# Kernel tuning notes

Hardware: AMD Instinct MI355X
Metric: run time of the kernel (lower is better)

The kernel has to match this reference:

```python
import jax, jax.numpy as jnp
import numpy as np

H = 256  # hidden_size
B = 8192  # batch
S = 1024  # seq_length


def setup_inputs() -> dict:
    key = jax.random.key(0)
    ks = jax.random.split(key, 12)
    lim_g = 1.0 / np.sqrt(1 + H)  # torch Linear default init bound, fan_in = 1+H
    lim_o = 1.0 / np.sqrt(H)
    def lin(k, out_dim, in_dim, lim):
        kw, kb = jax.random.split(k)
        W = jax.random.uniform(kw, (out_dim, in_dim), jnp.float32, -lim, lim)
        b = jax.random.uniform(kb, (out_dim,), jnp.float32, -lim, lim)
        return W, b
    Wf, bf = lin(ks[0], H, 1 + H, lim_g)
    Wi, bi = lin(ks[1], H, 1 + H, lim_g)
    Wc, bc = lin(ks[2], H, 1 + H, lim_g)
    Wo, bo = lin(ks[3], H, 1 + H, lim_g)
    Wout, bout = lin(ks[4], 1, H, lim_o)
    x = jax.random.normal(ks[5], (B, S), jnp.float32)
    return {"x": x, "Wf": Wf, "bf": bf, "Wi": Wi, "bi": bi,
            "Wc": Wc, "bc": bc, "Wo": Wo, "bo": bo,
            "Wout": Wout, "bout": bout}


def reference(x, Wf, bf, Wi, bi, Wc, bc, Wo, bo, Wout, bout):
    B_, S_ = x.shape
    H_ = Wf.shape[0]
    # Fuse the four gate linears into one GEMM per step (same math):
    Wall = jnp.concatenate([Wf, Wi, Wc, Wo], axis=0)      # [4H, 1+H]
    ball = jnp.concatenate([bf, bi, bc, bo], axis=0)      # [4H]

    def step(carry, xt):
        h, c = carry                                       # [B,H], [B,H]
        conc = jnp.concatenate([xt[:, None], h], axis=1)   # [B, 1+H]
        g = conc @ Wall.T + ball                           # [B, 4H]
        f, i, cs, o = jnp.split(g, 4, axis=1)
        c = jax.nn.sigmoid(f) * c + jax.nn.sigmoid(i) * jnp.tanh(cs)
        h = jax.nn.sigmoid(o) * jnp.tanh(c)
        return (h, c), None

    h0 = jnp.zeros((B_, H_), x.dtype)
    c0 = jnp.zeros((B_, H_), x.dtype)
    (h, _), _ = jax.lax.scan(step, (h0, c0), x.T)          # scan over seq axis
    out = h @ Wout.T + bout                                # [B, 1]
    return out.squeeze(-1)                                 # [B]
```

## Files before the change

kernel.cpp:

```cpp
#include <hip/hip_runtime.h>
#include <hip/hip_fp16.h>


typedef _Float16 f16x8 __attribute__((ext_vector_type(8)));
typedef float f32x4 __attribute__((ext_vector_type(4)));
typedef unsigned int u32;
typedef unsigned short u16;

#define WINT_OFF 0u
#define W0B_OFF  524288u
#define FLAG_OFF 528384u
#define PUB_OFF  1048576u

static __device__ __forceinline__ float fast_exp2(float x) {
#if __has_builtin(__builtin_amdgcn_exp2f)
  return __builtin_amdgcn_exp2f(x);
#else
  return exp2f(x);
#endif
}
static __device__ __forceinline__ float fast_rcp(float x) {
#if __has_builtin(__builtin_amdgcn_rcpf)
  return __builtin_amdgcn_rcpf(x);
#else
  return 1.0f / x;
#endif
}
static __device__ __forceinline__ u16 f16b(float f) {
  union { _Float16 h; u16 u; } cv; cv.h = (_Float16)f; return cv.u;
}
static __device__ __forceinline__ float h2f(u16 u) {
  union { u16 u; _Float16 h; } cv; cv.u = u; return (float)cv.h;
}
static __device__ __forceinline__ u16* pub_base(u16* pub, int set, int par,
                                                int pid, int half) {
  return pub + ((size_t)(((set * 2 + par) * 128 + pid) * 2 + half) << 12);
}

__global__ void lstm_prep(const float* __restrict__ Wf, const float* __restrict__ Wi,
                          const float* __restrict__ Wc, const float* __restrict__ Wo,
                          const float* __restrict__ bf_, const float* __restrict__ bi_,
                          const float* __restrict__ bc_, const float* __restrict__ bo_,
                          u16* __restrict__ Wint, u32* __restrict__ w0b) {
  int n = blockIdx.x;
  int k = threadIdx.x;
  int g = n >> 8, j = n & 255;
  const float* Ws = (g == 0) ? Wf : (g == 1) ? Wi : (g == 2) ? Wc : Wo;
  const float scale = (g == 2) ? 2.88539008f : 1.44269504f;
  Wint[n * 256 + k] = f16b(Ws[j * 257 + 1 + k] * scale);
  if (k == 0) {
    const float* bs = (g == 0) ? bf_ : (g == 1) ? bi_ : (g == 2) ? bc_ : bo_;
    w0b[n] = (u32)f16b(Ws[j * 257] * scale) | ((u32)f16b(bs[j] * scale) << 16);
  }
}

__global__ void lstm_zero(uint4* __restrict__ pub4, uint4* __restrict__ flags4,
                          float* __restrict__ out, const float* __restrict__ bout) {
  int idx = blockIdx.x * 256 + threadIdx.x;
  uint4 z = uint4{0, 0, 0, 0};
  if (idx < 131072) pub4[idx] = z;
  else if (idx < 262144) pub4[idx + 131072] = z;
  else if (idx < 264192) flags4[idx - 262144] = z;
  else { int o = idx - 264192; if (o < 8192) out[o] = bout[0]; }
}

__global__ __launch_bounds__(512, 2) void lstm_main(
    const u16* __restrict__ Wint, const u32* __restrict__ w0b,
    const float* __restrict__ x, const float* __restrict__ Wout,
    float* __restrict__ out, u16* __restrict__ pub, int* __restrict__ flags) {

  __shared__ __align__(16) u16 stg[2][2][4096];

  const int tid  = threadIdx.x;
  const int wv   = tid >> 6;
  const int lane = tid & 63;
  const int l15  = lane & 15;
  const int quad = lane >> 4;
  const int B    = blockIdx.x;
  const int mi   = (B >> 3) & 1;
  const int peer = B ^ 8;
  const int pid  = (B & 7) | ((B >> 4) << 3);
  const int rows0 = pid * 64;

  f16x8 wfrag[4][8];
#pragma unroll
  for (int g = 0; g < 4; ++g)
#pragma unroll
    for (int hm = 0; hm < 2; ++hm)
#pragma unroll
      for (int ktl = 0; ktl < 4; ++ktl) {
        int kbase = (hm == 0 ? mi : 1 - mi) * 128 + ktl * 32;
        wfrag[g][hm * 4 + ktl] = *(const f16x8*)(Wint +
            (size_t)(g * 256 + mi * 128 + wv * 16 + l15) * 256 + kbase + quad * 8);
      }
  float w0f[4][4], bsf[4][4];
#pragma unroll
  for (int g = 0; g < 4; ++g) {
    uint4 wv4 = *(const uint4*)(w0b + g * 256 + mi * 128 + wv * 16 + quad * 4);
    u32 pka[4] = {wv4.x, wv4.y, wv4.z, wv4.w};
#pragma unroll
    for (int r = 0; r < 4; ++r) {
      w0f[g][r] = h2f((u16)pka[r]);
      bsf[g][r] = h2f((u16)(pka[r] >> 16));
    }
  }

#pragma unroll
  for (int i = 0; i < 4; ++i) ((uint4*)stg)[tid + i * 512] = uint4{0, 0, 0, 0};

  float cst[2][2][4];
#pragma unroll
  for (int s = 0; s < 2; ++s)
#pragma unroll
    for (int bt = 0; bt < 2; ++bt)
#pragma unroll
      for (int r = 0; r < 4; ++r) cst[s][bt][r] = 0.0f;

  const float* xq = x + (size_t)rows0 * 1024;
  float xcur[2][2];
#pragma unroll
  for (int s = 0; s < 2; ++s)
#pragma unroll
    for (int bt = 0; bt < 2; ++bt)
      xcur[s][bt] = xq[(size_t)(s * 32 + bt * 16 + l15) * 1024];

  int* const myflag = flags + B * 32;
  int* const pfl    = flags + peer * 32;

  __syncthreads();

#pragma unroll 1
  for (int t = 0; t < 1024; ++t) {
#pragma unroll
    for (int s = 0; s < 2; ++s) {
      f32x4 acc[4][2];
#pragma unroll
      for (int g = 0; g < 4; ++g)
#pragma unroll
        for (int r = 0; r < 4; ++r) {
          acc[g][0][r] = xcur[s][0] * w0f[g][r] + bsf[g][r];
          acc[g][1][r] = xcur[s][1] * w0f[g][r] + bsf[g][r];
        }
#pragma unroll
      for (int bt = 0; bt < 2; ++bt)
        xcur[s][bt] = xq[(size_t)(s * 32 + bt * 16 + l15) * 1024 + ((t + 1) & 1023)];

#pragma unroll
      for (int hm = 0; hm < 2; ++hm)
#pragma unroll
        for (int ktl = 0; ktl < 4; ++ktl) {
          f16x8 bb[2];
#pragma unroll
          for (int bt = 0; bt < 2; ++bt) {
            int b = bt * 16 + l15;
            int cp = (ktl * 4 + quad) ^ (b & 15);
            bb[bt] = *(const f16x8*)(&stg[s][hm][0] + b * 128 + cp * 8);
          }
#pragma unroll
          for (int g = 0; g < 4; ++g)
#pragma unroll
            for (int bt = 0; bt < 2; ++bt)
              acc[g][bt] = __builtin_amdgcn_mfma_f32_16x16x32_f16(
                  wfrag[g][hm * 4 + ktl], bb[bt], acc[g][bt], 0, 0, 0);
        }

      const int tn = (s == 0) ? t : t + 1;
      if (tn < 1024) {
        while (__hip_atomic_load(pfl + (s ^ 1) * 16, __ATOMIC_RELAXED,
                                 __HIP_MEMORY_SCOPE_AGENT) < tn)
          __builtin_amdgcn_s_sleep(1);
        const u16* srcO = pub_base(pub, s ^ 1, tn & 1, pid, mi);
        const u16* srcP = pub_base(pub, s ^ 1, tn & 1, pid, 1 - mi);
        __builtin_amdgcn_global_load_lds(
            (const __attribute__((address_space(1))) u32*)(srcO + wv * 512 + lane * 8),
            (__attribute__((address_space(3))) u32*)(&stg[s ^ 1][0][wv * 512]), 16, 0, 0);
        __builtin_amdgcn_global_load_lds(
            (const __attribute__((address_space(1))) u32*)(srcP + wv * 512 + lane * 8),
            (__attribute__((address_space(3))) u32*)(&stg[s ^ 1][1][wv * 512]), 16, 0, 0);
      }

      u16* pb = pub_base(pub, s, (t + 1) & 1, pid, mi);
#pragma unroll
      for (int bt = 0; bt < 2; ++bt) {
        int b = bt * 16 + l15;
        u32 lo, hi;
        {
          float h0, h1, h2, h3;
#pragma unroll
          for (int r = 0; r < 4; ++r) {
            float fg = acc[0][bt][r], ig = acc[1][bt][r];
            float cg = acc[2][bt][r], og = acc[3][bt][r];
            float sf  = fast_rcp(1.0f + fast_exp2(-fg));
            float C   = fast_exp2(cg);
            float Ei  = fast_exp2(-ig);
            float itv = (C - 1.0f) * fast_rcp((1.0f + Ei) * (C + 1.0f));
            float c_  = sf * cst[s][bt][r] + itv;
            cst[s][bt][r] = c_;
            float C2  = fast_exp2(2.88539008f * c_);
            float th  = 1.0f - 2.0f * fast_rcp(1.0f + C2);
            float so  = fast_rcp(1.0f + fast_exp2(-og));
            float hv  = so * th;
            if (r == 0) h0 = hv; else if (r == 1) h1 = hv;
            else if (r == 2) h2 = hv; else h3 = hv;
          }
          lo = (u32)f16b(h0) | ((u32)f16b(h1) << 16);
          hi = (u32)f16b(h2) | ((u32)f16b(h3) << 16);
        }
        int c16 = wv * 2 + (quad >> 1);
        int cp  = c16 ^ (b & 15);
        *(uint2*)(pb + b * 128 + cp * 8 + (quad & 1) * 4) = uint2{lo, hi};
      }

      __syncthreads();
      if (tid == 0)
        __hip_atomic_store(myflag + s * 16, t + 1, __ATOMIC_RELAXED,
                           __HIP_MEMORY_SCOPE_AGENT);
    }
  }

  if (tid < 64) {
    int s = tid >> 5, b = tid & 31;
    const u16* pbase = pub_base(pub, s, 0, pid, mi);
    float a = 0.0f;
#pragma unroll
    for (int c = 0; c < 16; ++c) {
      f16x8 hv = *(const f16x8*)(pbase + b * 128 + ((c ^ (b & 15)) * 8));
#pragma unroll
      for (int e = 0; e < 8; ++e) a += (float)hv[e] * Wout[mi * 128 + c * 8 + e];
    }
    atomicAdd(&out[rows0 + s * 32 + b], a);
  }
}

extern "C" void kernel_launch(void* const* d_in, const int* in_sizes, int n_in,
                              void* d_out, int out_size, void* d_ws, size_t ws_size,
                              hipStream_t stream) {
  const float* x    = (const float*)d_in[0];
  const float* Wf   = (const float*)d_in[1];
  const float* bf_  = (const float*)d_in[2];
  const float* Wi   = (const float*)d_in[3];
  const float* bi_  = (const float*)d_in[4];
  const float* Wc   = (const float*)d_in[5];
  const float* bc_  = (const float*)d_in[6];
  const float* Wo   = (const float*)d_in[7];
  const float* bo_  = (const float*)d_in[8];
  const float* Wout = (const float*)d_in[9];
  const float* bout = (const float*)d_in[10];

  u16* Wint  = (u16*)((char*)d_ws + WINT_OFF);
  u32* w0b   = (u32*)((char*)d_ws + W0B_OFF);
  int* flags = (int*)((char*)d_ws + FLAG_OFF);
  u16* pub   = (u16*)((char*)d_ws + PUB_OFF);

  lstm_prep<<<1024, 256, 0, stream>>>(Wf, Wi, Wc, Wo, bf_, bi_, bc_, bo_, Wint, w0b);
  lstm_zero<<<1064, 256, 0, stream>>>((uint4*)pub, (uint4*)flags, (float*)d_out, bout);
  lstm_main<<<256, 512, 0, stream>>>(Wint, w0b, x, Wout, (float*)d_out, pub, flags);
}
```

Baseline: 4.704 ms.

## Split waves into MFMA and elementwise groups to overlap recurrent step phases

Result: slower. 5.439 ms (+15.6%).

```diff
diff --git a/kernel.cpp b/kernel.cpp
--- a/kernel.cpp
+++ b/kernel.cpp
@@ -69,13 +69,14 @@
     const float* __restrict__ x, const float* __restrict__ Wout,
     float* __restrict__ out, u16* __restrict__ pub, int* __restrict__ flags) {
 
-  __shared__ __align__(16) u16 stg[2][2][4096];
+  __shared__ __align__(16) u16 stg[2][2][2][4096];
 
   const int tid  = threadIdx.x;
   const int wv   = tid >> 6;
   const int lane = tid & 63;
   const int l15  = lane & 15;
   const int quad = lane >> 4;
+  const int grp  = (wv & 1) ^ ((wv >> 2) & 1);
   const int B    = blockIdx.x;
   const int mi   = (B >> 3) & 1;
   const int peer = B ^ 8;
@@ -106,7 +107,7 @@
   }
 
 #pragma unroll
-  for (int i = 0; i < 4; ++i) ((uint4*)stg)[tid + i * 512] = uint4{0, 0, 0, 0};
+  for (int i = 0; i < 8; ++i) ((uint4*)stg)[tid + i * 512] = uint4{0, 0, 0, 0};
 
   float cst[2][2][4];
 #pragma unroll
@@ -115,6 +116,8 @@
     for (int bt = 0; bt < 2; ++bt)
 #pragma unroll
       for (int r = 0; r < 4; ++r) cst[s][bt][r] = 0.0f;
+
+  f32x4 acc[4][2];
 
   const float* xq = x + (size_t)rows0 * 1024;
   float xcur[2][2];
@@ -129,94 +132,149 @@
 
   __syncthreads();
 
+#define DO_K(S, T, LEAD) do {                                                  \
+    const int par_ = (T) & 1;                                                  \
+    if (LEAD) {                                                                \
+      while (__hip_atomic_load(pfl + (S) * 16, __ATOMIC_RELAXED,               \
+                               __HIP_MEMORY_SCOPE_AGENT) < (T))                \
+        __builtin_amdgcn_s_sleep(1);                                           \
+      const u16* srcP_ = pub_base(pub, (S), par_, pid, 1 - mi);                \
+      u16* dst_ = &stg[S][par_][1][0];                                         \
+      _Pragma("unroll")                                                        \
+      for (int i_ = 0; i_ < 8; ++i_)                                           \
+        __builtin_amdgcn_global_load_lds(                                      \
+            (const __attribute__((address_space(1))) u32*)(srcP_ + i_ * 512 + lane * 8), \
+            (__attribute__((address_space(3))) u32*)(dst_ + i_ * 512), 16, 0, 0); \
+      __builtin_amdgcn_sched_barrier(0);                                       \
+    }                                                                          \
+    _Pragma("unroll")                                                          \
+    for (int g_ = 0; g_ < 4; ++g_)                                             \
+      _Pragma("unroll")                                                        \
+      for (int r_ = 0; r_ < 4; ++r_) {                                         \
+        acc[g_][0][r_] = xcur[S][0] * w0f[g_][r_] + bsf[g_][r_];               \
+        acc[g_][1][r_] = xcur[S][1] * w0f[g_][r_] + bsf[g_][r_];               \
+      }                                                                        \
+    _Pragma("unroll")                                                          \
+    for (int ktl_ = 0; ktl_ < 4; ++ktl_) {                                     \
+      f16x8 bb_[2];                                                            \
+      _Pragma("unroll")                                                        \
+      for (int bt_ = 0; bt_ < 2; ++bt_) {                                      \
+        int b_ = bt_ * 16 + l15;                                               \
+        int cp_ = (ktl_ * 4 + quad) ^ (b_ & 15);                               \
+        bb_[bt_] = *(const f16x8*)(&stg[S][par_][0][0] + b_ * 128 + cp_ * 8);  \
+      }                                                                        \
+      _Pragma("unroll")                                                        \
+      for (int g_ = 0; g_ < 4; ++g_)                                           \
+        _Pragma("unroll")                                                      \
+        for (int bt_ = 0; bt_ < 2; ++bt_)                                      \
+          acc[g_][bt_] = __builtin_amdgcn_mfma_f32_16x16x32_f16(               \
+              wfrag[g_][ktl_], bb_[bt_], acc[g_][bt_], 0, 0, 0);               \
+    }                                                                          \
+    if (LEAD) {                                                                \
+      asm volatile("s_waitcnt vmcnt(0)" ::: "memory");                         \
+      __builtin_amdgcn_sched_barrier(0);                                       \
+    }                                                                          \
+    _Pragma("unroll")                                                          \
+    for (int ktl_ = 0; ktl_ < 4; ++ktl_) {                                     \
+      f16x8 bb_[2];                                                            \
+      _Pragma("unroll")                                                        \
+      for (int bt_ = 0; bt_ < 2; ++bt_) {                                      \
+        int b_ = bt_ * 16 + l15;                                               \
+        int cp_ = (ktl_ * 4 + quad) ^ (b_ & 15);                               \
+        bb_[bt_] = *(const f16x8*)(&stg[S][par_][1][0] + b_ * 128 + cp_ * 8);  \
+      }                                                                        \
+      _Pragma("unroll")                                                        \
+      for (int g_ = 0; g_ < 4; ++g_)                                           \
+        _Pragma("unroll")                                                      \
+        for (int bt_ = 0; bt_ < 2; ++bt_)                                      \
+          acc[g_][bt_] = __builtin_amdgcn_mfma_f32_16x16x32_f16(               \
+              wfrag[g_][4 + ktl_], bb_[bt_], acc[g_][bt_], 0, 0, 0);           \
+    }                                                                          \
+  } while (0)
+
+#define DO_EW(S, TEW) do {                                                     \
+    const int parn_ = ((TEW) + 1) & 1;                                         \
+    u16* pb_ = pub_base(pub, (S), parn_, pid, mi);                             \
+    u16* lb_ = &stg[S][parn_][0][0];                                           \
+    _Pragma("unroll")                                                          \
+    for (int bt_ = 0; bt_ < 2; ++bt_) {                                        \
+      int b_ = bt_ * 16 + l15;                                                 \
+      u32 lo_, hi_;                                                            \
+      {                                                                        \
+        float h0_, h1_, h2_, h3_;                                              \
+        _Pragma("unroll")                                                      \
+        for (int r_ = 0; r_ < 4; ++r_) {                                       \
+          float fg_ = acc[0][bt_][r_], ig_ = acc[1][bt_][r_];                  \
+          float cg_ = acc[2][bt_][r_], og_ = acc[3][bt_][r_];                  \
+          float Ef_ = fast_exp2(-fg_);                                         \
+          float Ei_ = fast_exp2(-ig_);                                         \
+          float C_  = fast_exp2(cg_);                                          \
+          float X_  = 1.0f + Ef_;                                              \
+          float Y_  = (1.0f + Ei_) * (C_ + 1.0f);                              \
+          float num_ = cst[S][bt_][r_] * Y_ + (C_ - 1.0f) * X_;                \
+          float c2_  = num_ * fast_rcp(X_ * Y_);                               \
+          cst[S][bt_][r_] = c2_;                                               \
+          float cc_ = fminf(fmaxf(c2_, -40.0f), 40.0f);                        \
+          float T_  = fast_exp2(2.88539008f * cc_);                            \
+          float Eo_ = fast_exp2(-og_);                                         \
+          float hv_ = (T_ - 1.0f) * fast_rcp((1.0f + Eo_) * (T_ + 1.0f));      \
+          if (r_ == 0) h0_ = hv_; else if (r_ == 1) h1_ = hv_;                 \
+          else if (r_ == 2) h2_ = hv_; else h3_ = hv_;                         \
+        }                                                                      \
+        lo_ = (u32)f16b(h0_) | ((u32)f16b(h1_) << 16);                         \
+        hi_ = (u32)f16b(h2_) | ((u32)f16b(h3_) << 16);                         \
+      }                                                                        \
+      int c16_ = wv * 2 + (quad >> 1);                                         \
+      int off_ = b_ * 128 + (c16_ ^ (b_ & 15)) * 8 + (quad & 1) * 4;           \
+      *(uint2*)(lb_ + off_) = uint2{lo_, hi_};                                 \
+      *(uint2*)(pb_ + off_) = uint2{lo_, hi_};                                 \
+    }                                                                          \
+  } while (0)
+
 #pragma unroll 1
   for (int t = 0; t < 1024; ++t) {
-#pragma unroll
-    for (int s = 0; s < 2; ++s) {
-      f32x4 acc[4][2];
-#pragma unroll
-      for (int g = 0; g < 4; ++g)
-#pragma unroll
-        for (int r = 0; r < 4; ++r) {
-          acc[g][0][r] = xcur[s][0] * w0f[g][r] + bsf[g][r];
-          acc[g][1][r] = xcur[s][1] * w0f[g][r] + bsf[g][r];
-        }
-#pragma unroll
-      for (int bt = 0; bt < 2; ++bt)
-        xcur[s][bt] = xq[(size_t)(s * 32 + bt * 16 + l15) * 1024 + ((t + 1) & 1023)];
-
-#pragma unroll
-      for (int hm = 0; hm < 2; ++hm)
-#pragma unroll
-        for (int ktl = 0; ktl < 4; ++ktl) {
-          f16x8 bb[2];
-#pragma unroll
-          for (int bt = 0; bt < 2; ++bt) {
-            int b = bt * 16 + l15;
-            int cp = (ktl * 4 + quad) ^ (b & 15);
-            bb[bt] = *(const f16x8*)(&stg[s][hm][0] + b * 128 + cp * 8);
-          }
-#pragma unroll
-          for (int g = 0; g < 4; ++g)
-#pragma unroll
-            for (int bt = 0; bt < 2; ++bt)
-              acc[g][bt] = __builtin_amdgcn_mfma_f32_16x16x32_f16(
-                  wfrag[g][hm * 4 + ktl], bb[bt], acc[g][bt], 0, 0, 0);
-        }
-
-      const int tn = (s == 0) ? t : t + 1;
-      if (tn < 1024) {
-        while (__hip_atomic_load(pfl + (s ^ 1) * 16, __ATOMIC_RELAXED,
-                                 __HIP_MEMORY_SCOPE_AGENT) < tn)
-          __builtin_amdgcn_s_sleep(1);
-        const u16* srcO = pub_base(pub, s ^ 1, tn & 1, pid, mi);
-        const u16* srcP = pub_base(pub, s ^ 1, tn & 1, pid, 1 - mi);
-        __builtin_amdgcn_global_load_lds(
-            (const __attribute__((address_space(1))) u32*)(srcO + wv * 512 + lane * 8),
-            (__attribute__((address_space(3))) u32*)(&stg[s ^ 1][0][wv * 512]), 16, 0, 0);
-        __builtin_amdgcn_global_load_lds(
-            (const __attribute__((address_space(1))) u32*)(srcP + wv * 512 + lane * 8),
-            (__attribute__((address_space(3))) u32*)(&stg[s ^ 1][1][wv * 512]), 16, 0, 0);
-      }
-
-      u16* pb = pub_base(pub, s, (t + 1) & 1, pid, mi);
-#pragma unroll
-      for (int bt = 0; bt < 2; ++bt) {
-        int b = bt * 16 + l15;
-        u32 lo, hi;
-        {
-          float h0, h1, h2, h3;
-#pragma unroll
-          for (int r = 0; r < 4; ++r) {
-            float fg = acc[0][bt][r], ig = acc[1][bt][r];
-            float cg = acc[2][bt][r], og = acc[3][bt][r];
-            float sf  = fast_rcp(1.0f + fast_exp2(-fg));
-            float C   = fast_exp2(cg);
-            float Ei  = fast_exp2(-ig);
-            float itv = (C - 1.0f) * fast_rcp((1.0f + Ei) * (C + 1.0f));
-            float c_  = sf * cst[s][bt][r] + itv;
-            cst[s][bt][r] = c_;
-            float C2  = fast_exp2(2.88539008f * c_);
-            float th  = 1.0f - 2.0f * fast_rcp(1.0f + C2);
-            float so  = fast_rcp(1.0f + fast_exp2(-og));
-            float hv  = so * th;
-            if (r == 0) h0 = hv; else if (r == 1) h1 = hv;
-            else if (r == 2) h2 = hv; else h3 = hv;
-          }
-          lo = (u32)f16b(h0) | ((u32)f16b(h1) << 16);
-          hi = (u32)f16b(h2) | ((u32)f16b(h3) << 16);
-        }
-        int c16 = wv * 2 + (quad >> 1);
-        int cp  = c16 ^ (b & 15);
-        *(uint2*)(pb + b * 128 + cp * 8 + (quad & 1) * 4) = uint2{lo, hi};
-      }
-
-      __syncthreads();
-      if (tid == 0)
-        __hip_atomic_store(myflag + s * 16, t + 1, __ATOMIC_RELAXED,
-                           __HIP_MEMORY_SCOPE_AGENT);
-    }
+    if (grp == 0) {
+      DO_K(0, t, 1);
+    } else {
+      if (t > 0) DO_EW(1, t - 1);
+      xcur[1][0] = xq[(size_t)(32 + l15) * 1024 + t];
+      xcur[1][1] = xq[(size_t)(48 + l15) * 1024 + t];
+    }
+    __syncthreads();
+    if (tid == 0)
+      __hip_atomic_store(myflag + 16, t, __ATOMIC_RELAXED,
+                         __HIP_MEMORY_SCOPE_AGENT);
+
+    if (grp == 0) DO_EW(0, t);
+    else          DO_K(0, t, 0);
+    __syncthreads();
+
+    if (grp == 0) {
+      DO_K(1, t, 1);
+    } else {
+      DO_EW(0, t);
+      xcur[0][0] = xq[(size_t)(l15) * 1024 + ((t + 1) & 1023)];
+      xcur[0][1] = xq[(size_t)(16 + l15) * 1024 + ((t + 1) & 1023)];
+    }
+    __syncthreads();
+    if (tid == 0)
+      __hip_atomic_store(myflag + 0, t + 1, __ATOMIC_RELAXED,
+                         __HIP_MEMORY_SCOPE_AGENT);
+
+    if (grp == 0) {
+      DO_EW(1, t);
+      xcur[0][0] = xq[(size_t)(l15) * 1024 + ((t + 1) & 1023)];
+      xcur[0][1] = xq[(size_t)(16 + l15) * 1024 + ((t + 1) & 1023)];
+      xcur[1][0] = xq[(size_t)(32 + l15) * 1024 + ((t + 1) & 1023)];
+      xcur[1][1] = xq[(size_t)(48 + l15) * 1024 + ((t + 1) & 1023)];
+    } else {
+      DO_K(1, t, 0);
+    }
+    __syncthreads();
   }
+
+  if (grp == 1) DO_EW(1, 1023);
+  __syncthreads();
 
   if (tid < 64) {
     int s = tid >> 5, b = tid & 31;
@@ -230,6 +288,8 @@
     }
     atomicAdd(&out[rows0 + s * 32 + b], a);
   }
+#undef DO_K
+#undef DO_EW
 }
 
 extern "C" void kernel_launch(void* const* d_in, const int* in_sizes, int n_in,
```

## Split rows into four 16-row streams and interleave gate math with MFMA

Applied to the files above, without the earlier changes.

After: 5.736 ms. 1.22x slower.

```diff
diff --git a/kernel.cpp b/kernel.cpp
--- a/kernel.cpp
+++ b/kernel.cpp
@@ -34,7 +34,7 @@
 }
 static __device__ __forceinline__ u16* pub_base(u16* pub, int set, int par,
                                                 int pid, int half) {
-  return pub + ((size_t)(((set * 2 + par) * 128 + pid) * 2 + half) << 12);
+  return pub + ((size_t)(((set * 2 + par) * 128 + pid) * 2 + half) << 11);
 }
 
 __global__ void lstm_prep(const float* __restrict__ Wf, const float* __restrict__ Wi,
@@ -54,14 +54,11 @@
   }
 }
 
-__global__ void lstm_zero(uint4* __restrict__ pub4, uint4* __restrict__ flags4,
-                          float* __restrict__ out, const float* __restrict__ bout) {
+__global__ void lstm_zero(uint4* __restrict__ flags4, float* __restrict__ out,
+                          const float* __restrict__ bout) {
   int idx = blockIdx.x * 256 + threadIdx.x;
-  uint4 z = uint4{0, 0, 0, 0};
-  if (idx < 131072) pub4[idx] = z;
-  else if (idx < 262144) pub4[idx + 131072] = z;
-  else if (idx < 264192) flags4[idx - 262144] = z;
-  else { int o = idx - 264192; if (o < 8192) out[o] = bout[0]; }
+  if (idx < 2048) flags4[idx] = uint4{0, 0, 0, 0};
+  else if (idx < 10240) out[idx - 2048] = bout[0];
 }
 
 __global__ __launch_bounds__(512, 2) void lstm_main(
@@ -69,7 +66,7 @@
     const float* __restrict__ x, const float* __restrict__ Wout,
     float* __restrict__ out, u16* __restrict__ pub, int* __restrict__ flags) {
 
-  __shared__ __align__(16) u16 stg[2][2][4096];
+  __shared__ __align__(16) u16 stg[4][2][2][2048];
 
   const int tid  = threadIdx.x;
   const int wv   = tid >> 6;
@@ -106,130 +103,137 @@
   }
 
 #pragma unroll
-  for (int i = 0; i < 4; ++i) ((uint4*)stg)[tid + i * 512] = uint4{0, 0, 0, 0};
-
-  float cst[2][2][4];
-#pragma unroll
-  for (int s = 0; s < 2; ++s)
-#pragma unroll
-    for (int bt = 0; bt < 2; ++bt)
-#pragma unroll
-      for (int r = 0; r < 4; ++r) cst[s][bt][r] = 0.0f;
+  for (int i = 0; i < 8; ++i) ((uint4*)stg)[tid + i * 512] = uint4{0, 0, 0, 0};
+
+  float cst[4][4];
+#pragma unroll
+  for (int s = 0; s < 4; ++s)
+#pragma unroll
+    for (int r = 0; r < 4; ++r) cst[s][r] = 0.0f;
+
+  f32x4 acc[2][4];
 
   const float* xq = x + (size_t)rows0 * 1024;
-  float xcur[2][2];
-#pragma unroll
-  for (int s = 0; s < 2; ++s)
-#pragma unroll
-    for (int bt = 0; bt < 2; ++bt)
-      xcur[s][bt] = xq[(size_t)(s * 32 + bt * 16 + l15) * 1024];
+  float xcur[4];
+#pragma unroll
+  for (int s = 0; s < 4; ++s)
+    xcur[s] = xq[(size_t)(s * 16 + l15) * 1024];
 
   int* const myflag = flags + B * 32;
   int* const pfl    = flags + peer * 32;
 
   __syncthreads();
 
+#define KSLOT(A, S) {                                                          \
+    const int cp_ = (((S & 3) * 4 + quad) ^ l15);                              \
+    f16x8 bb_ = *(const f16x8*)(&stg[A][t & 1][(S) >> 2][0] + l15 * 128 + cp_ * 8); \
+    _Pragma("unroll")                                                          \
+    for (int g_ = 0; g_ < 4; ++g_)                                             \
+      acc[(A) & 1][g_] = __builtin_amdgcn_mfma_f32_16x16x32_f16(               \
+          wfrag[g_][S], bb_, acc[(A) & 1][g_], 0, 0, 0);                       \
+  }
+
+#define EWELEM(BS, R) {                                                        \
+    float fg_ = acc[(BS) & 1][0][R], ig_ = acc[(BS) & 1][1][R];                \
+    float cg_ = acc[(BS) & 1][2][R], og_ = acc[(BS) & 1][3][R];                \
+    float Ef_ = fast_exp2(-fg_);                                               \
+    float Ei_ = fast_exp2(-ig_);                                               \
+    float C_  = fast_exp2(cg_);                                                \
+    float X_  = 1.0f + Ef_;                                                    \
+    float Y_  = (1.0f + Ei_) * (C_ + 1.0f);                                    \
+    float num_ = cst[BS][R] * Y_ + (C_ - 1.0f) * X_;                           \
+    float c2_  = num_ * fast_rcp(X_ * Y_);                                     \
+    cst[BS][R] = c2_;                                                          \
+    float cc_ = fminf(fmaxf(c2_, -40.0f), 40.0f);                              \
+    float T_  = fast_exp2(2.88539008f * cc_);                                  \
+    float Eo_ = fast_exp2(-og_);                                               \
+    float hv_ = (T_ - 1.0f) * fast_rcp((1.0f + Eo_) * (T_ + 1.0f));            \
+    if ((R) == 0) h0_ = hv_; else if ((R) == 1) h1_ = hv_;                     \
+    else if ((R) == 2) h2_ = hv_; else h3_ = hv_;                              \
+  }
+
+#define SUBSTEP(A, BS, TEW, DC, TC, EWEN, DMAEN) do {                          \
+    const int tew_ = (TEW);                                                    \
+    const int tc_  = (TC);                                                     \
+    float h0_, h1_, h2_, h3_;                                                  \
+    if (DMAEN) {                                                               \
+      while (__hip_atomic_load(pfl + (DC) * 8, __ATOMIC_RELAXED,               \
+                               __HIP_MEMORY_SCOPE_AGENT) < tc_)                \
+        __builtin_amdgcn_s_sleep(1);                                           \
+      if (wv < 4) {                                                            \
+        const u16* src_ = pub_base(pub, DC, tc_ & 1, pid, 1 - mi) +            \
+                          wv * 512 + lane * 8;                                 \
+        __builtin_amdgcn_global_load_lds(                                      \
+            (const __attribute__((address_space(1))) u32*)src_,                \
+            (__attribute__((address_space(3))) u32*)(&stg[DC][tc_ & 1][1][wv * 512]), \
+            16, 0, 0);                                                         \
+      }                                                                        \
+    }                                                                          \
+    _Pragma("unroll")                                                          \
+    for (int g_ = 0; g_ < 4; ++g_)                                             \
+      _Pragma("unroll")                                                        \
+      for (int r_ = 0; r_ < 4; ++r_)                                           \
+        acc[(A) & 1][g_][r_] = xcur[A] * w0f[g_][r_] + bsf[g_][r_];            \
+    xcur[A] = xq[(size_t)((A) * 16 + l15) * 1024 + ((t + 1) & 1023)];          \
+    KSLOT(A, 0) KSLOT(A, 1)                                                    \
+    if (EWEN) { EWELEM(BS, 0) }                                                \
+    KSLOT(A, 2)                                                                \
+    if (EWEN) { EWELEM(BS, 1) }                                                \
+    KSLOT(A, 3)                                                                \
+    if (EWEN) { EWELEM(BS, 2) }                                                \
+    KSLOT(A, 4)                                                                \
+    if (EWEN) { EWELEM(BS, 3) }                                                \
+    KSLOT(A, 5)                                                                \
+    if (EWEN) {                                                                \
+      u32 lo_ = (u32)f16b(h0_) | ((u32)f16b(h1_) << 16);                       \
+      u32 hi_ = (u32)f16b(h2_) | ((u32)f16b(h3_) << 16);                       \
+      int c16_ = wv * 2 + (quad >> 1);                                         \
+      int off_ = l15 * 128 + ((c16_ ^ l15) * 8) + (quad & 1) * 4;              \
+      *(uint2*)(&stg[BS][(tew_ + 1) & 1][0][0] + off_) = uint2{lo_, hi_};      \
+      *(uint2*)(pub_base(pub, BS, (tew_ + 1) & 1, pid, mi) + off_) =           \
+          uint2{lo_, hi_};                                                     \
+    }                                                                          \
+    KSLOT(A, 6) KSLOT(A, 7)                                                    \
+    __syncthreads();                                                           \
+    if ((EWEN) && tid == 0)                                                    \
+      __hip_atomic_store(myflag + (BS) * 8, tew_ + 1, __ATOMIC_RELAXED,        \
+                         __HIP_MEMORY_SCOPE_AGENT);                            \
+  } while (0)
+
 #pragma unroll 1
   for (int t = 0; t < 1024; ++t) {
-#pragma unroll
-    for (int s = 0; s < 2; ++s) {
-      f32x4 acc[4][2];
-#pragma unroll
-      for (int g = 0; g < 4; ++g)
-#pragma unroll
-        for (int r = 0; r < 4; ++r) {
-          acc[g][0][r] = xcur[s][0] * w0f[g][r] + bsf[g][r];
-          acc[g][1][r] = xcur[s][1] * w0f[g][r] + bsf[g][r];
-        }
-#pragma unroll
-      for (int bt = 0; bt < 2; ++bt)
-        xcur[s][bt] = xq[(size_t)(s * 32 + bt * 16 + l15) * 1024 + ((t + 1) & 1023)];
-
-#pragma unroll
-      for (int hm = 0; hm < 2; ++hm)
-#pragma unroll
-        for (int ktl = 0; ktl < 4; ++ktl) {
-          f16x8 bb[2];
-#pragma unroll
-          for (int bt = 0; bt < 2; ++bt) {
-            int b = bt * 16 + l15;
-            int cp = (ktl * 4 + quad) ^ (b & 15);
-            bb[bt] = *(const f16x8*)(&stg[s][hm][0] + b * 128 + cp * 8);
-          }
-#pragma unroll
-          for (int g = 0; g < 4; ++g)
-#pragma unroll
-            for (int bt = 0; bt < 2; ++bt)
-              acc[g][bt] = __builtin_amdgcn_mfma_f32_16x16x32_f16(
-                  wfrag[g][hm * 4 + ktl], bb[bt], acc[g][bt], 0, 0, 0);
-        }
-
-      const int tn = (s == 0) ? t : t + 1;
-      if (tn < 1024) {
-        while (__hip_atomic_load(pfl + (s ^ 1) * 16, __ATOMIC_RELAXED,
-                                 __HIP_MEMORY_SCOPE_AGENT) < tn)
-          __builtin_amdgcn_s_sleep(1);
-        const u16* srcO = pub_base(pub, s ^ 1, tn & 1, pid, mi);
-        const u16* srcP = pub_base(pub, s ^ 1, tn & 1, pid, 1 - mi);
-        __builtin_amdgcn_global_load_lds(
-            (const __attribute__((address_space(1))) u32*)(srcO + wv * 512 + lane * 8),
-            (__attribute__((address_space(3))) u32*)(&stg[s ^ 1][0][wv * 512]), 16, 0, 0);
-        __builtin_amdgcn_global_load_lds(
-            (const __attribute__((address_space(1))) u32*)(srcP + wv * 512 + lane * 8),
-            (__attribute__((address_space(3))) u32*)(&stg[s ^ 1][1][wv * 512]), 16, 0, 0);
-      }
-
-      u16* pb = pub_base(pub, s, (t + 1) & 1, pid, mi);
-#pragma unroll
-      for (int bt = 0; bt < 2; ++bt) {
-        int b = bt * 16 + l15;
-        u32 lo, hi;
-        {
-          float h0, h1, h2, h3;
-#pragma unroll
-          for (int r = 0; r < 4; ++r) {
-            float fg = acc[0][bt][r], ig = acc[1][bt][r];
-            float cg = acc[2][bt][r], og = acc[3][bt][r];
-            float sf  = fast_rcp(1.0f + fast_exp2(-fg));
-            float C   = fast_exp2(cg);
-            float Ei  = fast_exp2(-ig);
-            float itv = (C - 1.0f) * fast_rcp((1.0f + Ei) * (C + 1.0f));
-            float c_  = sf * cst[s][bt][r] + itv;
-            cst[s][bt][r] = c_;
-            float C2  = fast_exp2(2.88539008f * c_);
-            float th  = 1.0f - 2.0f * fast_rcp(1.0f + C2);
-            float so  = fast_rcp(1.0f + fast_exp2(-og));
-            float hv  = so * th;
-            if (r == 0) h0 = hv; else if (r == 1) h1 = hv;
-            else if (r == 2) h2 = hv; else h3 = hv;
-          }
-          lo = (u32)f16b(h0) | ((u32)f16b(h1) << 16);
-          hi = (u32)f16b(h2) | ((u32)f16b(h3) << 16);
-        }
-        int c16 = wv * 2 + (quad >> 1);
-        int cp  = c16 ^ (b & 15);
-        *(uint2*)(pb + b * 128 + cp * 8 + (quad & 1) * 4) = uint2{lo, hi};
-      }
-
-      __syncthreads();
-      if (tid == 0)
-        __hip_atomic_store(myflag + s * 16, t + 1, __ATOMIC_RELAXED,
-                           __HIP_MEMORY_SCOPE_AGENT);
-    }
-  }
+    SUBSTEP(0, 3, t - 1, 1, t,     (t > 0), (t > 0));
+    SUBSTEP(1, 0, t,     2, t,     1,       (t > 0));
+    SUBSTEP(2, 1, t,     3, t,     1,       (t > 0));
+    SUBSTEP(3, 2, t,     0, t + 1, 1,       (t < 1023));
+  }
+
+  {
+    float h0_, h1_, h2_, h3_;
+    EWELEM(3, 0) EWELEM(3, 1) EWELEM(3, 2) EWELEM(3, 3)
+    u32 lo_ = (u32)f16b(h0_) | ((u32)f16b(h1_) << 16);
+    u32 hi_ = (u32)f16b(h2_) | ((u32)f16b(h3_) << 16);
+    int c16_ = wv * 2 + (quad >> 1);
+    int off_ = l15 * 128 + ((c16_ ^ l15) * 8) + (quad & 1) * 4;
+    *(uint2*)(pub_base(pub, 3, 0, pid, mi) + off_) = uint2{lo_, hi_};
+  }
+  __syncthreads();
 
   if (tid < 64) {
-    int s = tid >> 5, b = tid & 31;
+    int s = tid >> 4, b = tid & 15;
     const u16* pbase = pub_base(pub, s, 0, pid, mi);
     float a = 0.0f;
 #pragma unroll
     for (int c = 0; c < 16; ++c) {
-      f16x8 hv = *(const f16x8*)(pbase + b * 128 + ((c ^ (b & 15)) * 8));
+      f16x8 hv = *(const f16x8*)(pbase + b * 128 + ((c ^ b) * 8));
 #pragma unroll
       for (int e = 0; e < 8; ++e) a += (float)hv[e] * Wout[mi * 128 + c * 8 + e];
     }
-    atomicAdd(&out[rows0 + s * 32 + b], a);
-  }
+    atomicAdd(&out[rows0 + s * 16 + b], a);
+  }
+#undef SUBSTEP
+#undef KSLOT
+#undef EWELEM
 }
 
 extern "C" void kernel_launch(void* const* d_in, const int* in_sizes, int n_in,
@@ -253,6 +257,6 @@
   u16* pub   = (u16*)((char*)d_ws + PUB_OFF);
 
   lstm_prep<<<1024, 256, 0, stream>>>(Wf, Wi, Wc, Wo, bf_, bi_, bc_, bo_, Wint, w0b);
-  lstm_zero<<<1064, 256, 0, stream>>>((uint4*)pub, (uint4*)flags, (float*)d_out, bout);
+  lstm_zero<<<40, 256, 0, stream>>>((uint4*)flags, (float*)d_out, bout);
   lstm_main<<<256, 512, 0, stream>>>(Wint, w0b, x, Wout, (float*)d_out, pub, flags);
 }
```
